# Optimization experiments

Measured on AMD Instinct MI355X. Metric: run time of the kernel, lower is better.

Reference implementation:

```python
import jax, jax.numpy as jnp
import numpy as np

N = 8192          # tokens
CD = 512          # coarse_dim
FD = 512          # fine_dim
CB = 4096         # coarse codebook size
FB = 8192         # fine codebook size
COST = 0.25       # commitment cost
LRELU = 0.1
EPS = 1e-5


def _vq(x, emb):
    # squared-distance cdist: [n, K]
    d = jnp.sum(x * x, axis=1, keepdims=True) + jnp.sum(emb * emb, axis=1) - 2.0 * (x @ emb.T)
    idx = jnp.argmin(d, axis=1)          # temperature=1.0 (updates=0); scaling doesn't change argmin
    q = emb[idx]                          # gather == one-hot @ emb, without materializing one-hot
    e_loss = jnp.mean((jax.lax.stop_gradient(q) - x) ** 2)
    q_loss = jnp.mean((q - jax.lax.stop_gradient(x)) ** 2)
    loss = q_loss + COST * e_loss
    q_st = x + jax.lax.stop_gradient(q - x)   # straight-through
    return q_st, loss


def _mlp(x, w, b, g, be):
    # Linear (torch: x @ W.T + b) -> LayerNorm -> LeakyReLU(0.1)
    h = x @ w.T + b
    m = jnp.mean(h, axis=-1, keepdims=True)
    v = jnp.var(h, axis=-1, keepdims=True)
    h = (h - m) / jnp.sqrt(v + EPS) * g + be
    return jnp.where(h > 0, h, LRELU * h)


def setup_inputs() -> dict:
    key = jax.random.key(0)
    ks = jax.random.split(key, 6)
    xav_c = float(np.sqrt(6.0 / (CB + CD)))
    xav_f = float(np.sqrt(6.0 / (FB + FD)))
    lin_s = float(np.sqrt(1.0 / CD))
    return {
        'z': jax.random.normal(ks[0], (N, CD + FD), dtype=jnp.float32),
        'coarse_emb': jax.random.uniform(ks[1], (CB, CD), jnp.float32, -xav_c, xav_c),
        'fine_emb': jax.random.uniform(ks[2], (FB, FD), jnp.float32, -xav_f, xav_f),
        'w_c2f': jax.random.uniform(ks[3], (FD, CD), jnp.float32, -lin_s, lin_s),
        'b_c2f': jnp.zeros((FD,), jnp.float32),
        'g_c2f': jnp.ones((FD,), jnp.float32),
        'be_c2f': jnp.zeros((FD,), jnp.float32),
        'w_f2c': jax.random.uniform(ks[4], (CD, FD), jnp.float32, -lin_s, lin_s),
        'b_f2c': jnp.zeros((CD,), jnp.float32),
        'g_f2c': jnp.ones((CD,), jnp.float32),
        'be_f2c': jnp.zeros((CD,), jnp.float32),
        'gate_c_raw': jnp.float32(0.5),
        'gate_f_raw': jnp.float32(0.5),
    }


def reference(z, coarse_emb, fine_emb, w_c2f, b_c2f, g_c2f, be_c2f,
              w_f2c, b_f2c, g_f2c, be_f2c, gate_c_raw, gate_f_raw):
    split = z.shape[1] // 2
    z_coarse, z_fine = z[:, :split], z[:, split:]

    z_coarse_q, coarse_loss = _vq(z_coarse, coarse_emb)
    coarse_influence = _mlp(jax.lax.stop_gradient(z_coarse_q), w_c2f, b_c2f, g_c2f, be_c2f)
    gate_c = jax.nn.sigmoid(gate_c_raw)

    residual = z_fine - gate_c * coarse_influence
    z_fine_q, fine_loss = _vq(residual, fine_emb)

    fine_feedback = _mlp(jax.lax.stop_gradient(z_fine_q), w_f2c, b_f2c, g_f2c, be_f2c)
    gate_f = jax.nn.sigmoid(gate_f_raw)

    z_coarse_corrected = z_coarse_q + 0.1 * gate_f * fine_feedback
    z_fine_reconstructed = z_fine_q + gate_c * coarse_influence
    z_hierarchical = jnp.concatenate([z_coarse_corrected, z_fine_reconstructed], axis=1)
    vq_loss = coarse_loss + fine_loss
    return z_hierarchical, vq_loss
```

## Files before the change

### kernel.cpp

```cpp
#include <hip/hip_runtime.h>
#include <hip/hip_bf16.h>
#include <cstdint>
#include <cstddef>

#define KD 512

#define OFF_CN   0u
#define OFF_FN   16384u
#define OFF_ZN   49152u
#define OFF_RN   81920u
#define OFF_LOSS 114688u
#define OFF_AMC  114944u
#define OFF_AMF  180480u
#define OFF_CEH  246016u
#define OFF_CEL  4440320u
#define OFF_FEH  8634624u
#define OFF_FEL  17023232u
#define OFF_ZCH  25411840u
#define OFF_ZCL  33800448u
#define OFF_RH   42189056u
#define OFF_RL   50577664u
#define OFF_W1H  58966272u
#define OFF_W1L  59490560u
#define OFF_W2H  60014848u
#define OFF_W2L  60539136u
#define OFF_H    61063424u
#define OFF_INFL 77840640u


typedef __attribute__((ext_vector_type(8))) short bf16x8;
typedef __attribute__((ext_vector_type(4))) float f32x4;

__device__ __forceinline__ bf16x8 as_bf16x8(int4 v) {
  union { int4 i; bf16x8 b; } u; u.i = v; return u.b;
}

__device__ __forceinline__ float block_sum(float v, float* sred) {
#pragma unroll
  for (int off = 32; off > 0; off >>= 1) v += __shfl_down(v, off, 64);
  if ((threadIdx.x & 63) == 0) sred[threadIdx.x >> 6] = v;
  __syncthreads();
  float r = sred[0] + sred[1] + sred[2] + sred[3];
  __syncthreads();
  return r;
}

__device__ __forceinline__ float sigmoidf_(float x) { return 1.0f / (1.0f + expf(-x)); }

__device__ __forceinline__ void split_bf16(float v, __hip_bfloat16* hi, __hip_bfloat16* lo) {
  __hip_bfloat16 h = __float2bfloat16(v);
  *hi = h;
  *lo = __float2bfloat16(v - __bfloat162float(h));
}

__global__ __launch_bounds__(256) void prep(
    const float* __restrict__ ce, const float* __restrict__ fe, const float* __restrict__ z,
    const float* __restrict__ w1, const float* __restrict__ w2,
    float* __restrict__ cn, float* __restrict__ fn, float* __restrict__ zn,
    __hip_bfloat16* __restrict__ ceH, __hip_bfloat16* __restrict__ ceL,
    __hip_bfloat16* __restrict__ feH, __hip_bfloat16* __restrict__ feL,
    __hip_bfloat16* __restrict__ zcH, __hip_bfloat16* __restrict__ zcL,
    __hip_bfloat16* __restrict__ w1H, __hip_bfloat16* __restrict__ w1L,
    __hip_bfloat16* __restrict__ w2H, __hip_bfloat16* __restrict__ w2L,
    float* __restrict__ lossp) {
  __shared__ float sred[4];
  const int b = blockIdx.x, t = threadIdx.x;
  const float* src;
  float* nd = nullptr;
  __hip_bfloat16 *dh, *dl;
  int fragMode = 0;
  size_t row;
  if (b < 4096) {
    row = b; src = ce + row * KD; nd = cn + row; dh = ceH; dl = ceL; fragMode = 1;
  } else if (b < 12288) {
    row = b - 4096; src = fe + row * KD; nd = fn + row; dh = feH; dl = feL; fragMode = 1;
  } else if (b < 20480) {
    row = b - 12288; src = z + row * 1024; nd = zn + row; dh = zcH; dl = zcL;
  } else if (b < 20992) {
    row = b - 20480; src = w1 + row * KD; dh = w1H; dl = w1L;
  } else {
    row = b - 20992; src = w2 + row * KD; dh = w2H; dl = w2L;
  }
  float acc = 0.0f;
  if (fragMode) {
    float v0 = src[t], v1 = src[t + 256];
    acc = v0 * v0 + v1 * v1;
  } else {
#pragma unroll
    for (int j = 0; j < 2; ++j) {
      int c = t + j * 256;
      float v = src[c];
      acc += v * v;
      __hip_bfloat16 h, l;
      split_bf16(v, &h, &l);
      dh[row * KD + c] = h;
      dl[row * KD + c] = l;
    }
  }
  if (nd) {
    float s = block_sum(acc, sred);
    if (t == 0) nd[0] = s;
  } else {
    __syncthreads();
    __syncthreads();
  }
  if (fragMode && t < 64) {
    union { int4 i; __hip_bfloat16 s[8]; } ph, pl;
#pragma unroll
    for (int j = 0; j < 8; ++j) {
      float v = src[8 * t + j];
      split_bf16(v, &ph.s[j], &pl.s[j]);
    }
    const int chunkIdx = (int)(((row >> 4) * 16 + (t >> 2)) * 64 +
                               ((size_t)((t & 3) << 4) | (row & 15)));
    ((int4*)dh)[chunkIdx] = ph.i;
    ((int4*)dl)[chunkIdx] = pl.i;
  }
  if (b == 20480 && t == 0) lossp[0] = 0.0f;
}

__global__ __launch_bounds__(256) void vq6(
    const int4* __restrict__ AfH, const int4* __restrict__ AfL,
    const __hip_bfloat16* __restrict__ Bh, const __hip_bfloat16* __restrict__ Bl,
    const float* __restrict__ qn, const float* __restrict__ cn,
    unsigned long long* __restrict__ amin) {
  __shared__ __align__(16) __hip_bfloat16 sBh[2][128 * 32];
  __shared__ __align__(16) __hip_bfloat16 sBl[2][128 * 32];
  const int t = threadIdx.x;
  const int w = t >> 6, l = t & 63;
  const int rowTile = blockIdx.y << 7;
  const int colTile = blockIdx.x << 7;
  const int wr = (w >> 1) << 6;
  const int wc = (w & 1) << 6;

  const int srow = t >> 2;
  const int sb = t & 3;
  const int skE = sb << 3;
  const int swz = (sb ^ ((srow >> 1) & 3)) << 3;
  const int wOff0 = (srow << 5) + swz;
  const int wOff1 = ((srow + 64) << 5) + swz;
  const size_t br0 = (size_t)(colTile + srow) * KD;
  const size_t br1 = (size_t)(colTile + 64 + srow) * KD;

  const int fr = l & 15;
  const int q = l >> 4;

  int aB[4];
#pragma unroll
  for (int mt = 0; mt < 4; ++mt)
    aB[mt] = (((rowTile + wr + (mt << 4)) >> 4) << 10) + l;

  f32x4 acc[4][4];
#pragma unroll
  for (int i = 0; i < 4; ++i)
#pragma unroll
    for (int j = 0; j < 4; ++j) acc[i][j] = (f32x4){0.f, 0.f, 0.f, 0.f};

  int4 rBh0 = *(const int4*)(Bh + br0 + skE);
  int4 rBh1 = *(const int4*)(Bh + br1 + skE);
  int4 rBl0 = *(const int4*)(Bl + br0 + skE);
  int4 rBl1 = *(const int4*)(Bl + br1 + skE);
  int4 aH[4], aL[4];
#pragma unroll
  for (int mt = 0; mt < 4; ++mt) {
    aH[mt] = AfH[aB[mt]];
    aL[mt] = AfL[aB[mt]];
  }

  int p = 0;
  for (int kk = 0; kk < KD; kk += 32) {
    *(int4*)(sBh[p] + wOff0) = rBh0; *(int4*)(sBh[p] + wOff1) = rBh1;
    *(int4*)(sBl[p] + wOff0) = rBl0; *(int4*)(sBl[p] + wOff1) = rBl1;
    __syncthreads();

    bf16x8 afh[4], afl[4];
#pragma unroll
    for (int mt = 0; mt < 4; ++mt) {
      afh[mt] = as_bf16x8(aH[mt]);
      afl[mt] = as_bf16x8(aL[mt]);
    }

    const int nkc = (kk + 32 < KD) ? ((kk >> 5) + 1) : 0;
    const int nkE = nkc << 5;
    rBh0 = *(const int4*)(Bh + br0 + nkE + skE);
    rBh1 = *(const int4*)(Bh + br1 + nkE + skE);
    rBl0 = *(const int4*)(Bl + br0 + nkE + skE);
    rBl1 = *(const int4*)(Bl + br1 + nkE + skE);
#pragma unroll
    for (int mt = 0; mt < 4; ++mt) {
      aH[mt] = AfH[aB[mt] + (nkc << 6)];
      aL[mt] = AfL[aB[mt] + (nkc << 6)];
    }

    bf16x8 bfh[4], bfl[4];
#pragma unroll
    for (int nt = 0; nt < 4; ++nt) {
      const int rB = wc + (nt << 4) + fr;
      const int o = (rB << 5) + ((q ^ ((rB >> 1) & 3)) << 3);
      bfh[nt] = *(const bf16x8*)(sBh[p] + o);
      bfl[nt] = *(const bf16x8*)(sBl[p] + o);
    }
#pragma unroll
    for (int mt = 0; mt < 4; ++mt)
#pragma unroll
      for (int nt = 0; nt < 4; ++nt) {
        acc[mt][nt] = __builtin_amdgcn_mfma_f32_16x16x32_bf16(afh[mt], bfh[nt], acc[mt][nt], 0, 0, 0);
        acc[mt][nt] = __builtin_amdgcn_mfma_f32_16x16x32_bf16(afh[mt], bfl[nt], acc[mt][nt], 0, 0, 0);
        acc[mt][nt] = __builtin_amdgcn_mfma_f32_16x16x32_bf16(afl[mt], bfh[nt], acc[mt][nt], 0, 0, 0);
      }
    p ^= 1;
  }

#pragma unroll
  for (int nt = 0; nt < 4; ++nt) {
    const int query = colTile + wc + (nt << 4) + fr;
    const float xn = qn[query];
    unsigned long long key = ~0ULL;
#pragma unroll
    for (int mt = 0; mt < 4; ++mt) {
#pragma unroll
      for (int reg = 0; reg < 4; ++reg) {
        const int code = rowTile + wr + (mt << 4) + (q << 2) + reg;
        float d = (xn + cn[code]) - 2.0f * acc[mt][nt][reg];
        unsigned ub = __float_as_uint(d);
        ub = (ub & 0x80000000u) ? ~ub : (ub | 0x80000000u);
        unsigned long long k2 = ((unsigned long long)ub << 32) | (unsigned long long)(unsigned)code;
        if (k2 < key) key = k2;
      }
    }
    unsigned long long o1 = __shfl_xor(key, 16, 64);
    if (o1 < key) key = o1;
    unsigned long long o2 = __shfl_xor(key, 32, 64);
    if (o2 < key) key = o2;
    if (l < 16) atomicMin(amin + colTile + wc + (nt << 4) + l, key);
  }
}

__global__ __launch_bounds__(256) void mlp6(
    const int4* __restrict__ AfH, const int4* __restrict__ AfL,
    const unsigned long long* __restrict__ gather,
    const __hip_bfloat16* __restrict__ Bh, const __hip_bfloat16* __restrict__ Bl,
    const float* __restrict__ bias, float* __restrict__ C) {
  __shared__ __align__(16) __hip_bfloat16 sAh[128 * 32];
  __shared__ __align__(16) __hip_bfloat16 sAl[128 * 32];
  __shared__ __align__(16) __hip_bfloat16 sBh[128 * 32];
  __shared__ __align__(16) __hip_bfloat16 sBl[128 * 32];
  const int t = threadIdx.x;
  const int w = t >> 6, l = t & 63;
  const int rowTile = blockIdx.y << 7;
  const int colTile = blockIdx.x << 7;
  const int wr = (w >> 1) << 6;
  const int wc = (w & 1) << 6;

  const int srow = t >> 2;
  const int sb = t & 3;
  const int skE = sb << 3;
  const int swz = (sb ^ ((srow >> 1) & 3)) << 3;
  const int wOff0 = (srow << 5) + swz;
  const int wOff1 = ((srow + 64) << 5) + swz;

  unsigned i0 = ((const unsigned*)gather)[2 * (rowTile + srow)];
  unsigned i1 = ((const unsigned*)gather)[2 * (rowTile + 64 + srow)];
  const int a0 = (int)((i0 >> 4) << 10) + (sb << 4) + (int)(i0 & 15);
  const int a1 = (int)((i1 >> 4) << 10) + (sb << 4) + (int)(i1 & 15);
  const size_t br0 = (size_t)(colTile + srow) * KD;
  const size_t br1 = (size_t)(colTile + 64 + srow) * KD;

  const int fr = l & 15;
  const int q = l >> 4;
  const int foff = (q ^ ((fr >> 1) & 3)) << 3;

  f32x4 acc[4][4];
#pragma unroll
  for (int i = 0; i < 4; ++i)
#pragma unroll
    for (int j = 0; j < 4; ++j) acc[i][j] = (f32x4){0.f, 0.f, 0.f, 0.f};

  for (int kk = 0; kk < KD; kk += 32) {
    const int kc64 = (kk >> 5) << 6;
    int4 vAh0 = AfH[a0 + kc64];
    int4 vAh1 = AfH[a1 + kc64];
    int4 vAl0 = AfL[a0 + kc64];
    int4 vAl1 = AfL[a1 + kc64];
    int4 vBh0 = *(const int4*)(Bh + br0 + kk + skE);
    int4 vBh1 = *(const int4*)(Bh + br1 + kk + skE);
    int4 vBl0 = *(const int4*)(Bl + br0 + kk + skE);
    int4 vBl1 = *(const int4*)(Bl + br1 + kk + skE);
    __syncthreads();
    *(int4*)(sAh + wOff0) = vAh0; *(int4*)(sAh + wOff1) = vAh1;
    *(int4*)(sAl + wOff0) = vAl0; *(int4*)(sAl + wOff1) = vAl1;
    *(int4*)(sBh + wOff0) = vBh0; *(int4*)(sBh + wOff1) = vBh1;
    *(int4*)(sBl + wOff0) = vBl0; *(int4*)(sBl + wOff1) = vBl1;
    __syncthreads();

    bf16x8 afh[4], afl[4], bfh[4], bfl[4];
#pragma unroll
    for (int mt = 0; mt < 4; ++mt) {
      const int rA = wr + (mt << 4) + fr;
      const int o = (rA << 5) + ((q ^ ((rA >> 1) & 3)) << 3);
      afh[mt] = *(const bf16x8*)(sAh + o);
      afl[mt] = *(const bf16x8*)(sAl + o);
    }
#pragma unroll
    for (int nt = 0; nt < 4; ++nt) {
      const int rB = wc + (nt << 4) + fr;
      const int o = (rB << 5) + ((q ^ ((rB >> 1) & 3)) << 3);
      bfh[nt] = *(const bf16x8*)(sBh + o);
      bfl[nt] = *(const bf16x8*)(sBl + o);
    }
#pragma unroll
    for (int mt = 0; mt < 4; ++mt)
#pragma unroll
      for (int nt = 0; nt < 4; ++nt) {
        acc[mt][nt] = __builtin_amdgcn_mfma_f32_16x16x32_bf16(afh[mt], bfh[nt], acc[mt][nt], 0, 0, 0);
        acc[mt][nt] = __builtin_amdgcn_mfma_f32_16x16x32_bf16(afh[mt], bfl[nt], acc[mt][nt], 0, 0, 0);
        acc[mt][nt] = __builtin_amdgcn_mfma_f32_16x16x32_bf16(afl[mt], bfh[nt], acc[mt][nt], 0, 0, 0);
      }
  }

  const int quad = l >> 4;
#pragma unroll
  for (int mt = 0; mt < 4; ++mt) {
#pragma unroll
    for (int reg = 0; reg < 4; ++reg) {
      const int row = rowTile + wr + (mt << 4) + (quad << 2) + reg;
#pragma unroll
      for (int nt = 0; nt < 4; ++nt) {
        const int col = colTile + wc + (nt << 4) + fr;
        C[(size_t)row * KD + col] = acc[mt][nt][reg] + bias[col];
      }
    }
  }
}

__global__ __launch_bounds__(256) void ln_residual(
    const float* __restrict__ h, const float* __restrict__ g, const float* __restrict__ be,
    const float* __restrict__ z, const float* __restrict__ gRaw,
    __hip_bfloat16* __restrict__ infl, float* __restrict__ rn,
    __hip_bfloat16* __restrict__ rH, __hip_bfloat16* __restrict__ rL) {
  __shared__ float sred[4];
  const int row = blockIdx.x, t = threadIdx.x;
  const size_t base = (size_t)row * KD;
  float h0 = h[base + t], h1 = h[base + t + 256];
  float m = block_sum(h0 + h1, sred) * (1.0f / 512.0f);
  float d0 = h0 - m, d1 = h1 - m;
  float var = block_sum(d0 * d0 + d1 * d1, sred) * (1.0f / 512.0f);
  float sq = sqrtf(var + 1e-5f);
  float gc = sigmoidf_(gRaw[0]);
  float v0 = d0 / sq * g[t] + be[t];
  float v1 = d1 / sq * g[t + 256] + be[t + 256];
  v0 = v0 > 0.0f ? v0 : 0.1f * v0;
  v1 = v1 > 0.0f ? v1 : 0.1f * v1;
  infl[base + t] = __float2bfloat16(v0);
  infl[base + t + 256] = __float2bfloat16(v1);
  float zf0 = z[(size_t)row * 1024 + 512 + t];
  float zf1 = z[(size_t)row * 1024 + 512 + t + 256];
  float r0 = zf0 - gc * v0, r1 = zf1 - gc * v1;
  __hip_bfloat16 hh, ll;
  split_bf16(r0, &hh, &ll);
  rH[base + t] = hh; rL[base + t] = ll;
  split_bf16(r1, &hh, &ll);
  rH[base + t + 256] = hh; rL[base + t + 256] = ll;
  float rs = block_sum(r0 * r0 + r1 * r1, sred);
  if (t == 0) rn[row] = rs;
}

__global__ __launch_bounds__(256) void finalize(
    const float* __restrict__ h, const float* __restrict__ g, const float* __restrict__ be,
    const __hip_bfloat16* __restrict__ infl,
    const unsigned long long* __restrict__ amc, const unsigned long long* __restrict__ amf,
    const float* __restrict__ z, const float* __restrict__ ce, const float* __restrict__ fe,
    const float* __restrict__ gcRaw, const float* __restrict__ gfRaw,
    float* __restrict__ out, float* __restrict__ lossp) {
  __shared__ float sred[4];
  const int row = blockIdx.x, t = threadIdx.x;
  const size_t base = (size_t)row * KD;
  float h0 = h[base + t], h1 = h[base + t + 256];
  float m = block_sum(h0 + h1, sred) * (1.0f / 512.0f);
  float d0 = h0 - m, d1 = h1 - m;
  float var = block_sum(d0 * d0 + d1 * d1, sred) * (1.0f / 512.0f);
  float sq = sqrtf(var + 1e-5f);
  float fb0 = d0 / sq * g[t] + be[t];
  float fb1 = d1 / sq * g[t + 256] + be[t + 256];
  fb0 = fb0 > 0.0f ? fb0 : 0.1f * fb0;
  fb1 = fb1 > 0.0f ? fb1 : 0.1f * fb1;
  float gc = sigmoidf_(gcRaw[0]);
  float gf = sigmoidf_(gfRaw[0]);
  unsigned ic = (unsigned)(amc[row] & 0xffffffffULL);
  unsigned ifx = (unsigned)(amf[row] & 0xffffffffULL);
  float loc = 0.0f;
#pragma unroll
  for (int j = 0; j < 2; ++j) {
    int c = t + j * 256;
    float fb = j ? fb1 : fb0;
    float qc = ce[(size_t)ic * KD + c];
    float qf = fe[(size_t)ifx * KD + c];
    float zc = z[(size_t)row * 1024 + c];
    float zf = z[(size_t)row * 1024 + 512 + c];
    float fl = __bfloat162float(infl[base + c]);
    out[(size_t)row * 1024 + c] = qc + 0.1f * gf * fb;
    out[(size_t)row * 1024 + 512 + c] = qf + gc * fl;
    float dc = qc - zc;
    float res = zf - gc * fl;
    float df = qf - res;
    loc += dc * dc + df * df;
  }
  float ls = block_sum(loc, sred);
  if (t == 0) atomicAdd(lossp, ls);
}

__global__ void loss_write(const float* __restrict__ lossp, float* __restrict__ out) {
  out[0] = 1.25f * lossp[0] / (8192.0f * 512.0f);
}

extern "C" void kernel_launch(void* const* d_in, const int* in_sizes, int n_in,
                              void* d_out, int out_size, void* d_ws, size_t ws_size,
                              hipStream_t stream) {
  const float* z      = (const float*)d_in[0];
  const float* ce     = (const float*)d_in[1];
  const float* fe     = (const float*)d_in[2];
  const float* w_c2f  = (const float*)d_in[3];
  const float* b_c2f  = (const float*)d_in[4];
  const float* g_c2f  = (const float*)d_in[5];
  const float* be_c2f = (const float*)d_in[6];
  const float* w_f2c  = (const float*)d_in[7];
  const float* b_f2c  = (const float*)d_in[8];
  const float* g_f2c  = (const float*)d_in[9];
  const float* be_f2c = (const float*)d_in[10];
  const float* gcRaw  = (const float*)d_in[11];
  const float* gfRaw  = (const float*)d_in[12];
  float* out = (float*)d_out;
  char* ws = (char*)d_ws;

  float* cn = (float*)(ws + OFF_CN);
  float* fn = (float*)(ws + OFF_FN);
  float* zn = (float*)(ws + OFF_ZN);
  float* rn = (float*)(ws + OFF_RN);
  float* lossp = (float*)(ws + OFF_LOSS);
  unsigned long long* amc = (unsigned long long*)(ws + OFF_AMC);
  unsigned long long* amf = (unsigned long long*)(ws + OFF_AMF);
  __hip_bfloat16* ceH = (__hip_bfloat16*)(ws + OFF_CEH);
  __hip_bfloat16* ceL = (__hip_bfloat16*)(ws + OFF_CEL);
  __hip_bfloat16* feH = (__hip_bfloat16*)(ws + OFF_FEH);
  __hip_bfloat16* feL = (__hip_bfloat16*)(ws + OFF_FEL);
  __hip_bfloat16* zcH = (__hip_bfloat16*)(ws + OFF_ZCH);
  __hip_bfloat16* zcL = (__hip_bfloat16*)(ws + OFF_ZCL);
  __hip_bfloat16* rH  = (__hip_bfloat16*)(ws + OFF_RH);
  __hip_bfloat16* rL  = (__hip_bfloat16*)(ws + OFF_RL);
  __hip_bfloat16* w1H = (__hip_bfloat16*)(ws + OFF_W1H);
  __hip_bfloat16* w1L = (__hip_bfloat16*)(ws + OFF_W1L);
  __hip_bfloat16* w2H = (__hip_bfloat16*)(ws + OFF_W2H);
  __hip_bfloat16* w2L = (__hip_bfloat16*)(ws + OFF_W2L);
  float* h = (float*)(ws + OFF_H);
  __hip_bfloat16* infl = (__hip_bfloat16*)(ws + OFF_INFL);

  hipMemsetAsync(ws + OFF_AMC, 0xFF, 131072, stream);

  prep<<<21504, 256, 0, stream>>>(ce, fe, z, w_c2f, w_f2c, cn, fn, zn,
                                  ceH, ceL, feH, feL, zcH, zcL,
                                  w1H, w1L, w2H, w2L, lossp);

  vq6<<<dim3(64, 32), 256, 0, stream>>>((const int4*)ceH, (const int4*)ceL,
                                        zcH, zcL, zn, cn, amc);

  mlp6<<<dim3(4, 64), 256, 0, stream>>>((const int4*)ceH, (const int4*)ceL, amc,
                                        w1H, w1L, b_c2f, h);

  ln_residual<<<8192, 256, 0, stream>>>(h, g_c2f, be_c2f, z, gcRaw, infl, rn, rH, rL);

  vq6<<<dim3(64, 64), 256, 0, stream>>>((const int4*)feH, (const int4*)feL,
                                        rH, rL, rn, fn, amf);

  mlp6<<<dim3(4, 64), 256, 0, stream>>>((const int4*)feH, (const int4*)feL, amf,
                                        w2H, w2L, b_f2c, h);

  finalize<<<8192, 256, 0, stream>>>(h, g_f2c, be_f2c, infl, amc, amf, z, ce, fe,
                                     gcRaw, gfRaw, out, lossp);
  loss_write<<<1, 1, 0, stream>>>(lossp, out + (size_t)8192 * 1024);
}
```

Before: 637.9 us.

## Widen VQ tiles to 256 codes per block, preswizzle MLP weights, slim prep

```diff
diff --git a/kernel.cpp b/kernel.cpp
--- a/kernel.cpp
+++ b/kernel.cpp
@@ -63,78 +63,75 @@
     __hip_bfloat16* __restrict__ w1H, __hip_bfloat16* __restrict__ w1L,
     __hip_bfloat16* __restrict__ w2H, __hip_bfloat16* __restrict__ w2L,
     float* __restrict__ lossp) {
-  __shared__ float sred[4];
   const int b = blockIdx.x, t = threadIdx.x;
-  const float* src;
-  float* nd = nullptr;
-  __hip_bfloat16 *dh, *dl;
-  int fragMode = 0;
-  size_t row;
-  if (b < 4096) {
-    row = b; src = ce + row * KD; nd = cn + row; dh = ceH; dl = ceL; fragMode = 1;
-  } else if (b < 12288) {
-    row = b - 4096; src = fe + row * KD; nd = fn + row; dh = feH; dl = feL; fragMode = 1;
-  } else if (b < 20480) {
-    row = b - 12288; src = z + row * 1024; nd = zn + row; dh = zcH; dl = zcL;
-  } else if (b < 20992) {
-    row = b - 20480; src = w1 + row * KD; dh = w1H; dl = w1L;
+  const int sub = t >> 6;
+  const int L = t & 63;
+  union { int4 i; __hip_bfloat16 s[8]; } ph, pl;
+  float acc = 0.0f;
+
+  if (b < 3072) {
+    int r = 4 * b + sub;
+    const float* src;
+    __hip_bfloat16 *dh, *dl;
+    float* np_;
+    int row;
+    if (r < 4096) { row = r; src = ce + (size_t)row * KD; dh = ceH; dl = ceL; np_ = cn + row; }
+    else { row = r - 4096; src = fe + (size_t)row * KD; dh = feH; dl = feL; np_ = fn + row; }
+    float4 v0 = *(const float4*)(src + 8 * L);
+    float4 v1 = *(const float4*)(src + 8 * L + 4);
+    float vv[8] = {v0.x, v0.y, v0.z, v0.w, v1.x, v1.y, v1.z, v1.w};
+#pragma unroll
+    for (int j = 0; j < 8; ++j) { acc += vv[j] * vv[j]; split_bf16(vv[j], &ph.s[j], &pl.s[j]); }
+    const int ci = ((row >> 4) * 16 + (L >> 2)) * 64 + ((L & 3) << 4) + (row & 15);
+    ((int4*)dh)[ci] = ph.i;
+    ((int4*)dl)[ci] = pl.i;
+#pragma unroll
+    for (int off = 32; off > 0; off >>= 1) acc += __shfl_down(acc, off, 64);
+    if (L == 0) np_[0] = acc;
+  } else if (b < 5120) {
+    int r = 4 * (b - 3072) + sub;
+    const float* src = z + (size_t)r * 1024;
+    float4 v0 = *(const float4*)(src + 8 * L);
+    float4 v1 = *(const float4*)(src + 8 * L + 4);
+    float vv[8] = {v0.x, v0.y, v0.z, v0.w, v1.x, v1.y, v1.z, v1.w};
+#pragma unroll
+    for (int j = 0; j < 8; ++j) { acc += vv[j] * vv[j]; split_bf16(vv[j], &ph.s[j], &pl.s[j]); }
+    ((int4*)zcH)[(size_t)r * 64 + L] = ph.i;
+    ((int4*)zcL)[(size_t)r * 64 + L] = pl.i;
+#pragma unroll
+    for (int off = 32; off > 0; off >>= 1) acc += __shfl_down(acc, off, 64);
+    if (L == 0) zn[r] = acc;
   } else {
-    row = b - 20992; src = w2 + row * KD; dh = w2H; dl = w2L;
-  }
-  float acc = 0.0f;
-  if (fragMode) {
-    float v0 = src[t], v1 = src[t + 256];
-    acc = v0 * v0 + v1 * v1;
-  } else {
-#pragma unroll
-    for (int j = 0; j < 2; ++j) {
-      int c = t + j * 256;
-      float v = src[c];
-      acc += v * v;
-      __hip_bfloat16 h, l;
-      split_bf16(v, &h, &l);
-      dh[row * KD + c] = h;
-      dl[row * KD + c] = l;
-    }
-  }
-  if (nd) {
-    float s = block_sum(acc, sred);
-    if (t == 0) nd[0] = s;
-  } else {
-    __syncthreads();
-    __syncthreads();
-  }
-  if (fragMode && t < 64) {
-    union { int4 i; __hip_bfloat16 s[8]; } ph, pl;
-#pragma unroll
-    for (int j = 0; j < 8; ++j) {
-      float v = src[8 * t + j];
-      split_bf16(v, &ph.s[j], &pl.s[j]);
-    }
-    const int chunkIdx = (int)(((row >> 4) * 16 + (t >> 2)) * 64 +
-                               ((size_t)((t & 3) << 4) | (row & 15)));
-    ((int4*)dh)[chunkIdx] = ph.i;
-    ((int4*)dl)[chunkIdx] = pl.i;
-  }
-  if (b == 20480 && t == 0) lossp[0] = 0.0f;
-}
-
-__global__ __launch_bounds__(256) void vq6(
+    int r = 4 * (b - 5120) + sub;
+    const float* src;
+    __hip_bfloat16 *dh, *dl;
+    int row;
+    if (r < 512) { row = r; src = w1 + (size_t)row * KD; dh = w1H; dl = w1L; }
+    else { row = r - 512; src = w2 + (size_t)row * KD; dh = w2H; dl = w2L; }
+    float4 v0 = *(const float4*)(src + 8 * L);
+    float4 v1 = *(const float4*)(src + 8 * L + 4);
+    float vv[8] = {v0.x, v0.y, v0.z, v0.w, v1.x, v1.y, v1.z, v1.w};
+#pragma unroll
+    for (int j = 0; j < 8; ++j) split_bf16(vv[j], &ph.s[j], &pl.s[j]);
+    const int ci = ((row >> 4) * 16 + (L >> 2)) * 64 + ((L & 3) << 4) + (row & 15);
+    ((int4*)dh)[ci] = ph.i;
+    ((int4*)dl)[ci] = pl.i;
+    if (b == 5120 && t == 0) lossp[0] = 0.0f;
+  }
+}
+
+__global__ __launch_bounds__(256) void vq7(
     const int4* __restrict__ AfH, const int4* __restrict__ AfL,
     const __hip_bfloat16* __restrict__ Bh, const __hip_bfloat16* __restrict__ Bl,
     const float* __restrict__ qn, const float* __restrict__ cn,
     unsigned long long* __restrict__ amin) {
   __shared__ __align__(16) __hip_bfloat16 sBh[2][128 * 32];
   __shared__ __align__(16) __hip_bfloat16 sBl[2][128 * 32];
-  const int t = threadIdx.x;
-  const int w = t >> 6, l = t & 63;
-  const int rowTile = blockIdx.y << 7;
+  const int t = threadIdx.x, w = t >> 6, l = t & 63;
   const int colTile = blockIdx.x << 7;
-  const int wr = (w >> 1) << 6;
-  const int wc = (w & 1) << 6;
-
-  const int srow = t >> 2;
-  const int sb = t & 3;
+  const int codeBase = (blockIdx.y << 8) + (w << 6);
+
+  const int srow = t >> 2, sb = t & 3;
   const int skE = sb << 3;
   const int swz = (sb ^ ((srow >> 1) & 3)) << 3;
   const int wOff0 = (srow << 5) + swz;
@@ -142,19 +139,17 @@
   const size_t br0 = (size_t)(colTile + srow) * KD;
   const size_t br1 = (size_t)(colTile + 64 + srow) * KD;
 
-  const int fr = l & 15;
-  const int q = l >> 4;
+  const int fr = l & 15, q = l >> 4;
 
   int aB[4];
 #pragma unroll
-  for (int mt = 0; mt < 4; ++mt)
-    aB[mt] = (((rowTile + wr + (mt << 4)) >> 4) << 10) + l;
-
-  f32x4 acc[4][4];
+  for (int mt = 0; mt < 4; ++mt) aB[mt] = ((codeBase >> 4) + mt) * 1024 + l;
+
+  f32x4 acc[4][8];
 #pragma unroll
   for (int i = 0; i < 4; ++i)
 #pragma unroll
-    for (int j = 0; j < 4; ++j) acc[i][j] = (f32x4){0.f, 0.f, 0.f, 0.f};
+    for (int j = 0; j < 8; ++j) acc[i][j] = (f32x4){0.f, 0.f, 0.f, 0.f};
 
   int4 rBh0 = *(const int4*)(Bh + br0 + skE);
   int4 rBh1 = *(const int4*)(Bh + br1 + skE);
@@ -162,10 +157,7 @@
   int4 rBl1 = *(const int4*)(Bl + br1 + skE);
   int4 aH[4], aL[4];
 #pragma unroll
-  for (int mt = 0; mt < 4; ++mt) {
-    aH[mt] = AfH[aB[mt]];
-    aL[mt] = AfL[aB[mt]];
-  }
+  for (int mt = 0; mt < 4; ++mt) { aH[mt] = AfH[aB[mt]]; aL[mt] = AfL[aB[mt]]; }
 
   int p = 0;
   for (int kk = 0; kk < KD; kk += 32) {
@@ -175,10 +167,7 @@
 
     bf16x8 afh[4], afl[4];
 #pragma unroll
-    for (int mt = 0; mt < 4; ++mt) {
-      afh[mt] = as_bf16x8(aH[mt]);
-      afl[mt] = as_bf16x8(aL[mt]);
-    }
+    for (int mt = 0; mt < 4; ++mt) { afh[mt] = as_bf16x8(aH[mt]); afl[mt] = as_bf16x8(aL[mt]); }
 
     const int nkc = (kk + 32 < KD) ? ((kk >> 5) + 1) : 0;
     const int nkE = nkc << 5;
@@ -192,35 +181,32 @@
       aL[mt] = AfL[aB[mt] + (nkc << 6)];
     }
 
-    bf16x8 bfh[4], bfl[4];
-#pragma unroll
-    for (int nt = 0; nt < 4; ++nt) {
-      const int rB = wc + (nt << 4) + fr;
+#pragma unroll
+    for (int nt = 0; nt < 8; ++nt) {
+      const int rB = (nt << 4) + fr;
       const int o = (rB << 5) + ((q ^ ((rB >> 1) & 3)) << 3);
-      bfh[nt] = *(const bf16x8*)(sBh[p] + o);
-      bfl[nt] = *(const bf16x8*)(sBl[p] + o);
-    }
-#pragma unroll
-    for (int mt = 0; mt < 4; ++mt)
-#pragma unroll
-      for (int nt = 0; nt < 4; ++nt) {
-        acc[mt][nt] = __builtin_amdgcn_mfma_f32_16x16x32_bf16(afh[mt], bfh[nt], acc[mt][nt], 0, 0, 0);
-        acc[mt][nt] = __builtin_amdgcn_mfma_f32_16x16x32_bf16(afh[mt], bfl[nt], acc[mt][nt], 0, 0, 0);
-        acc[mt][nt] = __builtin_amdgcn_mfma_f32_16x16x32_bf16(afl[mt], bfh[nt], acc[mt][nt], 0, 0, 0);
+      bf16x8 bfh = *(const bf16x8*)(sBh[p] + o);
+      bf16x8 bfl = *(const bf16x8*)(sBl[p] + o);
+#pragma unroll
+      for (int mt = 0; mt < 4; ++mt) {
+        acc[mt][nt] = __builtin_amdgcn_mfma_f32_16x16x32_bf16(afh[mt], bfh, acc[mt][nt], 0, 0, 0);
+        acc[mt][nt] = __builtin_amdgcn_mfma_f32_16x16x32_bf16(afh[mt], bfl, acc[mt][nt], 0, 0, 0);
+        acc[mt][nt] = __builtin_amdgcn_mfma_f32_16x16x32_bf16(afl[mt], bfh, acc[mt][nt], 0, 0, 0);
       }
+    }
     p ^= 1;
   }
 
 #pragma unroll
-  for (int nt = 0; nt < 4; ++nt) {
-    const int query = colTile + wc + (nt << 4) + fr;
+  for (int nt = 0; nt < 8; ++nt) {
+    const int query = colTile + (nt << 4) + fr;
     const float xn = qn[query];
     unsigned long long key = ~0ULL;
 #pragma unroll
     for (int mt = 0; mt < 4; ++mt) {
 #pragma unroll
       for (int reg = 0; reg < 4; ++reg) {
-        const int code = rowTile + wr + (mt << 4) + (q << 2) + reg;
+        const int code = codeBase + (mt << 4) + (q << 2) + reg;
         float d = (xn + cn[code]) - 2.0f * acc[mt][nt][reg];
         unsigned ub = __float_as_uint(d);
         ub = (ub & 0x80000000u) ? ~ub : (ub | 0x80000000u);
@@ -232,43 +218,37 @@
     if (o1 < key) key = o1;
     unsigned long long o2 = __shfl_xor(key, 32, 64);
     if (o2 < key) key = o2;
-    if (l < 16) atomicMin(amin + colTile + wc + (nt << 4) + l, key);
-  }
-}
-
-__global__ __launch_bounds__(256) void mlp6(
+    if (l < 16) atomicMin(amin + colTile + (nt << 4) + l, key);
+  }
+}
+
+__global__ __launch_bounds__(256) void mlp7(
     const int4* __restrict__ AfH, const int4* __restrict__ AfL,
     const unsigned long long* __restrict__ gather,
-    const __hip_bfloat16* __restrict__ Bh, const __hip_bfloat16* __restrict__ Bl,
+    const int4* __restrict__ WfH, const int4* __restrict__ WfL,
     const float* __restrict__ bias, float* __restrict__ C) {
-  __shared__ __align__(16) __hip_bfloat16 sAh[128 * 32];
-  __shared__ __align__(16) __hip_bfloat16 sAl[128 * 32];
-  __shared__ __align__(16) __hip_bfloat16 sBh[128 * 32];
-  __shared__ __align__(16) __hip_bfloat16 sBl[128 * 32];
-  const int t = threadIdx.x;
-  const int w = t >> 6, l = t & 63;
+  __shared__ __align__(16) __hip_bfloat16 sAh[2][128 * 32];
+  __shared__ __align__(16) __hip_bfloat16 sAl[2][128 * 32];
+  const int t = threadIdx.x, w = t >> 6, l = t & 63;
   const int rowTile = blockIdx.y << 7;
   const int colTile = blockIdx.x << 7;
   const int wr = (w >> 1) << 6;
   const int wc = (w & 1) << 6;
 
-  const int srow = t >> 2;
-  const int sb = t & 3;
-  const int skE = sb << 3;
+  const int srow = t >> 2, sb = t & 3;
   const int swz = (sb ^ ((srow >> 1) & 3)) << 3;
   const int wOff0 = (srow << 5) + swz;
   const int wOff1 = ((srow + 64) << 5) + swz;
-
-  unsigned i0 = ((const unsigned*)gather)[2 * (rowTile + srow)];
-  unsigned i1 = ((const unsigned*)gather)[2 * (rowTile + 64 + srow)];
-  const int a0 = (int)((i0 >> 4) << 10) + (sb << 4) + (int)(i0 & 15);
-  const int a1 = (int)((i1 >> 4) << 10) + (sb << 4) + (int)(i1 & 15);
-  const size_t br0 = (size_t)(colTile + srow) * KD;
-  const size_t br1 = (size_t)(colTile + 64 + srow) * KD;
-
-  const int fr = l & 15;
-  const int q = l >> 4;
-  const int foff = (q ^ ((fr >> 1) & 3)) << 3;
+  const unsigned i0 = ((const unsigned*)gather)[2 * (rowTile + srow)];
+  const unsigned i1 = ((const unsigned*)gather)[2 * (rowTile + 64 + srow)];
+  const int a0 = (int)((i0 >> 4) * 1024) + (sb << 4) + (int)(i0 & 15);
+  const int a1 = (int)((i1 >> 4) * 1024) + (sb << 4) + (int)(i1 & 15);
+
+  const int fr = l & 15, q = l >> 4;
+
+  int bB[4];
+#pragma unroll
+  for (int nt = 0; nt < 4; ++nt) bB[nt] = (((colTile + wc) >> 4) + nt) * 1024 + l;
 
   f32x4 acc[4][4];
 #pragma unroll
@@ -276,46 +256,44 @@
 #pragma unroll
     for (int j = 0; j < 4; ++j) acc[i][j] = (f32x4){0.f, 0.f, 0.f, 0.f};
 
+  int4 rAh0 = AfH[a0], rAh1 = AfH[a1], rAl0 = AfL[a0], rAl1 = AfL[a1];
+  int4 bH[4], bL[4];
+#pragma unroll
+  for (int nt = 0; nt < 4; ++nt) { bH[nt] = WfH[bB[nt]]; bL[nt] = WfL[bB[nt]]; }
+
+  int p = 0;
   for (int kk = 0; kk < KD; kk += 32) {
-    const int kc64 = (kk >> 5) << 6;
-    int4 vAh0 = AfH[a0 + kc64];
-    int4 vAh1 = AfH[a1 + kc64];
-    int4 vAl0 = AfL[a0 + kc64];
-    int4 vAl1 = AfL[a1 + kc64];
-    int4 vBh0 = *(const int4*)(Bh + br0 + kk + skE);
-    int4 vBh1 = *(const int4*)(Bh + br1 + kk + skE);
-    int4 vBl0 = *(const int4*)(Bl + br0 + kk + skE);
-    int4 vBl1 = *(const int4*)(Bl + br1 + kk + skE);
+    *(int4*)(sAh[p] + wOff0) = rAh0; *(int4*)(sAh[p] + wOff1) = rAh1;
+    *(int4*)(sAl[p] + wOff0) = rAl0; *(int4*)(sAl[p] + wOff1) = rAl1;
     __syncthreads();
-    *(int4*)(sAh + wOff0) = vAh0; *(int4*)(sAh + wOff1) = vAh1;
-    *(int4*)(sAl + wOff0) = vAl0; *(int4*)(sAl + wOff1) = vAl1;
-    *(int4*)(sBh + wOff0) = vBh0; *(int4*)(sBh + wOff1) = vBh1;
-    *(int4*)(sBl + wOff0) = vBl0; *(int4*)(sBl + wOff1) = vBl1;
-    __syncthreads();
-
-    bf16x8 afh[4], afl[4], bfh[4], bfl[4];
+
+    bf16x8 bfh[4], bfl[4];
+#pragma unroll
+    for (int nt = 0; nt < 4; ++nt) { bfh[nt] = as_bf16x8(bH[nt]); bfl[nt] = as_bf16x8(bL[nt]); }
+
+    const int nkc = (kk + 32 < KD) ? ((kk >> 5) + 1) : 0;
+    rAh0 = AfH[a0 + nkc * 64]; rAh1 = AfH[a1 + nkc * 64];
+    rAl0 = AfL[a0 + nkc * 64]; rAl1 = AfL[a1 + nkc * 64];
+#pragma unroll
+    for (int nt = 0; nt < 4; ++nt) {
+      bH[nt] = WfH[bB[nt] + (nkc << 6)];
+      bL[nt] = WfL[bB[nt] + (nkc << 6)];
+    }
+
 #pragma unroll
     for (int mt = 0; mt < 4; ++mt) {
       const int rA = wr + (mt << 4) + fr;
       const int o = (rA << 5) + ((q ^ ((rA >> 1) & 3)) << 3);
-      afh[mt] = *(const bf16x8*)(sAh + o);
-      afl[mt] = *(const bf16x8*)(sAl + o);
-    }
-#pragma unroll
-    for (int nt = 0; nt < 4; ++nt) {
-      const int rB = wc + (nt << 4) + fr;
-      const int o = (rB << 5) + ((q ^ ((rB >> 1) & 3)) << 3);
-      bfh[nt] = *(const bf16x8*)(sBh + o);
-      bfl[nt] = *(const bf16x8*)(sBl + o);
-    }
-#pragma unroll
-    for (int mt = 0; mt < 4; ++mt)
+      bf16x8 afh = *(const bf16x8*)(sAh[p] + o);
+      bf16x8 afl = *(const bf16x8*)(sAl[p] + o);
 #pragma unroll
       for (int nt = 0; nt < 4; ++nt) {
-        acc[mt][nt] = __builtin_amdgcn_mfma_f32_16x16x32_bf16(afh[mt], bfh[nt], acc[mt][nt], 0, 0, 0);
-        acc[mt][nt] = __builtin_amdgcn_mfma_f32_16x16x32_bf16(afh[mt], bfl[nt], acc[mt][nt], 0, 0, 0);
-        acc[mt][nt] = __builtin_amdgcn_mfma_f32_16x16x32_bf16(afl[mt], bfh[nt], acc[mt][nt], 0, 0, 0);
+        acc[mt][nt] = __builtin_amdgcn_mfma_f32_16x16x32_bf16(afh, bfh[nt], acc[mt][nt], 0, 0, 0);
+        acc[mt][nt] = __builtin_amdgcn_mfma_f32_16x16x32_bf16(afh, bfl[nt], acc[mt][nt], 0, 0, 0);
+        acc[mt][nt] = __builtin_amdgcn_mfma_f32_16x16x32_bf16(afl, bfh[nt], acc[mt][nt], 0, 0, 0);
       }
+    }
+    p ^= 1;
   }
 
   const int quad = l >> 4;
@@ -456,23 +434,23 @@
 
   hipMemsetAsync(ws + OFF_AMC, 0xFF, 131072, stream);
 
-  prep<<<21504, 256, 0, stream>>>(ce, fe, z, w_c2f, w_f2c, cn, fn, zn,
-                                  ceH, ceL, feH, feL, zcH, zcL,
-                                  w1H, w1L, w2H, w2L, lossp);
-
-  vq6<<<dim3(64, 32), 256, 0, stream>>>((const int4*)ceH, (const int4*)ceL,
+  prep<<<5376, 256, 0, stream>>>(ce, fe, z, w_c2f, w_f2c, cn, fn, zn,
+                                 ceH, ceL, feH, feL, zcH, zcL,
+                                 w1H, w1L, w2H, w2L, lossp);
+
+  vq7<<<dim3(64, 16), 256, 0, stream>>>((const int4*)ceH, (const int4*)ceL,
                                         zcH, zcL, zn, cn, amc);
 
-  mlp6<<<dim3(4, 64), 256, 0, stream>>>((const int4*)ceH, (const int4*)ceL, amc,
-                                        w1H, w1L, b_c2f, h);
+  mlp7<<<dim3(4, 64), 256, 0, stream>>>((const int4*)ceH, (const int4*)ceL, amc,
+                                        (const int4*)w1H, (const int4*)w1L, b_c2f, h);
 
   ln_residual<<<8192, 256, 0, stream>>>(h, g_c2f, be_c2f, z, gcRaw, infl, rn, rH, rL);
 
-  vq6<<<dim3(64, 64), 256, 0, stream>>>((const int4*)feH, (const int4*)feL,
+  vq7<<<dim3(64, 32), 256, 0, stream>>>((const int4*)feH, (const int4*)feL,
                                         rH, rL, rn, fn, amf);
 
-  mlp6<<<dim3(4, 64), 256, 0, stream>>>((const int4*)feH, (const int4*)feL, amf,
-                                        w2H, w2L, b_f2c, h);
+  mlp7<<<dim3(4, 64), 256, 0, stream>>>((const int4*)feH, (const int4*)feL, amf,
+                                        (const int4*)w2H, (const int4*)w2L, b_f2c, h);
 
   finalize<<<8192, 256, 0, stream>>>(h, g_f2c, be_f2c, infl, amc, amf, z, ce, fe,
                                      gcRaw, gfRaw, out, lossp);
```

Measured after the change: 676.1 us. +6.0%, slower.
